# Kernel optimization log

Hardware: AMD Instinct MI355X
Metric: run time of the kernel (lower is better)

## Reference

```python
import jax, jax.numpy as jnp
import numpy as np

B, S, ENC_H, DEC_H, ATTN = 64, 2048, 512, 512, 512


def setup_inputs() -> dict:
    key = jax.random.key(0)
    k1, k2, k3, k4, k5 = jax.random.split(key, 5)
    enc_outputs = jax.random.normal(k1, (B, S, ENC_H), dtype=jnp.float32)
    dec_hidden = jax.random.normal(k2, (B, DEC_H), dtype=jnp.float32)
    # nn.Linear(in, out, bias=False): weight shape [out, in]; y = x @ W.T
    s_enc = 1.0 / np.sqrt(ENC_H)
    s_dec = 1.0 / np.sqrt(DEC_H)
    s_v = 1.0 / np.sqrt(ATTN)
    W_enc = jax.random.uniform(k3, (ATTN, ENC_H), minval=-s_enc, maxval=s_enc, dtype=jnp.float32)
    W_dec = jax.random.uniform(k4, (ATTN, DEC_H), minval=-s_dec, maxval=s_dec, dtype=jnp.float32)
    v = jax.random.uniform(k5, (1, ATTN), minval=-s_v, maxval=s_v, dtype=jnp.float32)
    return {"enc_outputs": enc_outputs, "dec_hidden": dec_hidden,
            "W_enc": W_enc, "W_dec": W_dec, "v": v}


def reference(enc_outputs, dec_hidden, W_enc, W_dec, v):
    # enc_proj: [B,S,A], dec_proj: [B,1,A]
    enc_proj = jnp.einsum('bse,ae->bsa', enc_outputs, W_enc)
    dec_proj = jnp.einsum('bd,ad->ba', dec_hidden, W_dec)[:, None, :]
    score = jnp.einsum('bsa,a->bs', jnp.tanh(enc_proj + dec_proj), v[0])  # [B,S]
    attn_weights = jax.nn.softmax(score, axis=1)
    context = jnp.einsum('bs,bse->be', attn_weights, enc_outputs)  # [B,ENC_H]
    return (context, attn_weights)
```

## Files before the change

### kernel.cpp

```cpp
#include <hip/hip_runtime.h>
#include <hip/hip_bf16.h>

#define B_N 64
#define S_N 2048
#define E_N 512
#define A_N 512

typedef __bf16 bf16x8 __attribute__((ext_vector_type(8)));
typedef float  f32x4  __attribute__((ext_vector_type(4)));

__device__ __forceinline__ unsigned int f2bfu(float f) {
  return (unsigned int)__builtin_bit_cast(unsigned short, (__bf16)f);
}

__global__ __launch_bounds__(256) void k_pack(const float* __restrict__ W,
                                              unsigned short* __restrict__ Wp) {
  const int pk = blockIdx.x * 256 + threadIdx.x;
  const int l = pk & 63, k32 = (pk >> 6) & 15, c = pk >> 10;
  const int ln = l & 15, q = l >> 4;
  const int a = c * 16 + ln, k = k32 * 32 + q * 8;
  const float* src = W + (size_t)a * E_N + k;
  const float4 u = *(const float4*)src;
  const float4 w = *(const float4*)(src + 4);
  uint4 o;
  o.x = f2bfu(u.x) | (f2bfu(u.y) << 16);
  o.y = f2bfu(u.z) | (f2bfu(u.w) << 16);
  o.z = f2bfu(w.x) | (f2bfu(w.y) << 16);
  o.w = f2bfu(w.z) | (f2bfu(w.w) << 16);
  *(uint4*)(Wp + (size_t)pk * 8) = o;
}

__global__ __launch_bounds__(256) void k_decproj(const float* __restrict__ dh,
                                                 const float* __restrict__ Wd,
                                                 float* __restrict__ decp) {
  const int b = blockIdx.x, tid = threadIdx.x;
  __shared__ float h[E_N];
  h[tid] = dh[b * E_N + tid];
  h[tid + 256] = dh[b * E_N + 256 + tid];
  __syncthreads();
  for (int a = tid; a < A_N; a += 256) {
    const float* wr = Wd + (size_t)a * E_N;
    float s = 0.f;
    #pragma unroll 8
    for (int e = 0; e < E_N; e += 4) {
      const float4 w4 = *(const float4*)(wr + e);
      s += w4.x * h[e] + w4.y * h[e + 1] + w4.z * h[e + 2] + w4.w * h[e + 3];
    }
    decp[b * A_N + a] = s;
  }
}

#define LDS_A   65536
#define RED_OFF LDS_A
#define LDS_TOT (LDS_A + 8 * 64 * 4)

__device__ __forceinline__ int a_off(int r, int kb) {
  return r * 1024 + (kb ^ ((r & 7) << 4));
}

__global__ __launch_bounds__(512, 4) void k_scores(
    const float* __restrict__ enc, const unsigned short* __restrict__ Wp,
    const float* __restrict__ decp, const float* __restrict__ vvec,
    float* __restrict__ scores) {
  __shared__ __align__(16) unsigned char lds[LDS_TOT];
  const int tid = threadIdx.x;
  const int lane = tid & 63, wv = tid >> 6, q = lane >> 4, ln = lane & 15;
  const int row0 = blockIdx.x * 64;
  const int b = row0 >> 11;
  const bf16x8* __restrict__ Wp16 = (const bf16x8*)Wp;

  float vv[4], dp[4];
  #pragma unroll
  for (int nt = 0; nt < 4; ++nt) {
    const int a = wv * 64 + nt * 16 + ln;
    vv[nt] = vvec[a];
    dp[nt] = decp[b * A_N + a];
  }

  {
    const float* srow = enc + (size_t)(row0 + wv * 8) * E_N + lane * 8;
    #pragma unroll 2
    for (int r8 = 0; r8 < 8; ++r8) {
      const float4 u = *(const float4*)(srow + (size_t)r8 * E_N);
      const float4 w = *(const float4*)(srow + (size_t)r8 * E_N + 4);
      uint4 o;
      o.x = f2bfu(u.x) | (f2bfu(u.y) << 16);
      o.y = f2bfu(u.z) | (f2bfu(u.w) << 16);
      o.z = f2bfu(w.x) | (f2bfu(w.y) << 16);
      o.w = f2bfu(w.z) | (f2bfu(w.w) << 16);
      *(uint4*)(lds + a_off(wv * 8 + r8, lane * 16)) = o;
    }
  }
  __syncthreads();

  f32x4 acc[4][4] = {};
  #pragma unroll 1
  for (int kss = 0; kss < 16; ++kss) {
    bf16x8 bfr[4], afr[4];
    #pragma unroll
    for (int nt = 0; nt < 4; ++nt)
      bfr[nt] = Wp16[(size_t)((wv * 4 + nt) * 16 + kss) * 64 + lane];
    #pragma unroll
    for (int mt = 0; mt < 4; ++mt)
      afr[mt] = *(const bf16x8*)(lds + a_off(mt * 16 + ln, kss * 64 + q * 16));
    #pragma unroll
    for (int mt = 0; mt < 4; ++mt)
      #pragma unroll
      for (int nt = 0; nt < 4; ++nt)
        acc[mt][nt] = __builtin_amdgcn_mfma_f32_16x16x32_bf16(
            afr[mt], bfr[nt], acc[mt][nt], 0, 0, 0);
  }

  float part[4][4] = {};
  #pragma unroll
  for (int mt = 0; mt < 4; ++mt)
    #pragma unroll
    for (int nt = 0; nt < 4; ++nt)
      #pragma unroll
      for (int r = 0; r < 4; ++r) {
        float x = acc[mt][nt][r] + dp[nt];
        x = fminf(9.f, fmaxf(-9.f, x));
        const float ex = __expf(2.f * x);
        part[mt][r] = fmaf(__fdividef(ex - 1.f, ex + 1.f), vv[nt], part[mt][r]);
      }
  float* red = (float*)(lds + RED_OFF);
  #pragma unroll
  for (int mt = 0; mt < 4; ++mt)
    #pragma unroll
    for (int r = 0; r < 4; ++r) {
      float s = part[mt][r];
      s += __shfl_xor(s, 1);
      s += __shfl_xor(s, 2);
      s += __shfl_xor(s, 4);
      s += __shfl_xor(s, 8);
      if (ln == 0) red[wv * 64 + mt * 16 + q * 4 + r] = s;
    }
  __syncthreads();
  if (tid < 64) {
    float s = 0.f;
    #pragma unroll
    for (int w8 = 0; w8 < 8; ++w8) s += red[w8 * 64 + tid];
    scores[row0 + tid] = s;
  }
}

__global__ __launch_bounds__(256) void k_softmax(const float* __restrict__ scores,
                                                 float* __restrict__ attn) {
  const int b = blockIdx.x, tid = threadIdx.x;
  float l[8];
  float mx = -3.4e38f;
  #pragma unroll
  for (int i = 0; i < 8; ++i) {
    l[i] = scores[b * S_N + i * 256 + tid];
    mx = fmaxf(mx, l[i]);
  }
  #pragma unroll
  for (int m = 1; m < 64; m <<= 1) mx = fmaxf(mx, __shfl_xor(mx, m));
  __shared__ float sred[8];
  if ((tid & 63) == 0) sred[tid >> 6] = mx;
  __syncthreads();
  mx = fmaxf(fmaxf(sred[0], sred[1]), fmaxf(sred[2], sred[3]));
  float se = 0.f;
  #pragma unroll
  for (int i = 0; i < 8; ++i) { l[i] = __expf(l[i] - mx); se += l[i]; }
  #pragma unroll
  for (int m = 1; m < 64; m <<= 1) se += __shfl_xor(se, m);
  if ((tid & 63) == 0) sred[4 + (tid >> 6)] = se;
  __syncthreads();
  se = sred[4] + sred[5] + sred[6] + sred[7];
  const float inv = 1.f / se;
  #pragma unroll
  for (int i = 0; i < 8; ++i) attn[b * S_N + i * 256 + tid] = l[i] * inv;
}

__global__ __launch_bounds__(512) void k_context(const float* __restrict__ enc,
                                                 const float* __restrict__ attn,
                                                 float* __restrict__ ctx) {
  const int blk = blockIdx.x;
  const int b = blk >> 2, eq = blk & 3;
  const int tid = threadIdx.x;
  const int te = tid & 31, sg = tid >> 5;
  const int e0 = eq * 128 + te * 4;
  const float* ep = enc + (size_t)b * S_N * E_N + e0;
  const float* wp = attn + b * S_N;
  f32x4 acc = {0.f, 0.f, 0.f, 0.f};
  const int s0 = sg * 128;
  #pragma unroll 4
  for (int s = s0; s < s0 + 128; ++s) {
    const float w = wp[s];
    const f32x4 ev = *(const f32x4*)(ep + (size_t)s * E_N);
    acc += w * ev;
  }
  __shared__ f32x4 red[16][32];
  red[sg][te] = acc;
  __syncthreads();
  if (sg == 0) {
    f32x4 t = red[0][te];
    #pragma unroll
    for (int g = 1; g < 16; ++g) t += red[g][te];
    *(f32x4*)(ctx + (size_t)b * E_N + e0) = t;
  }
}

extern "C" void kernel_launch(void* const* d_in, const int* in_sizes, int n_in,
                              void* d_out, int out_size, void* d_ws, size_t ws_size,
                              hipStream_t stream) {
  const float* enc = (const float*)d_in[0];
  const float* dh  = (const float*)d_in[1];
  const float* We  = (const float*)d_in[2];
  const float* Wd  = (const float*)d_in[3];
  const float* v   = (const float*)d_in[4];

  float* out_ctx  = (float*)d_out;
  float* out_attn = out_ctx + B_N * E_N;

  float* scores = (float*)d_ws;
  float* decp   = scores + B_N * S_N;
  unsigned short* Wp = (unsigned short*)(decp + B_N * A_N);

  k_pack   <<<128, 256, 0, stream>>>(We, Wp);
  k_decproj<<<B_N, 256, 0, stream>>>(dh, Wd, decp);
  k_scores <<<(B_N * S_N) / 64, 512, 0, stream>>>(enc, Wp, decp, v, scores);
  k_softmax<<<B_N, 256, 0, stream>>>(scores, out_attn);
  k_context<<<B_N * 4, 512, 0, stream>>>(enc, out_attn, out_ctx);
}
```

Before: 193.4 us.

## Make score kernel persistent with W slice resident in LDS and split-A partials

```diff
diff --git a/kernel.cpp b/kernel.cpp
--- a/kernel.cpp
+++ b/kernel.cpp
@@ -5,6 +5,7 @@
 #define S_N 2048
 #define E_N 512
 #define A_N 512
+#define SPN (B_N * S_N)
 
 typedef __bf16 bf16x8 __attribute__((ext_vector_type(8)));
 typedef float  f32x4  __attribute__((ext_vector_type(4)));
@@ -50,39 +51,46 @@
   }
 }
 
-#define LDS_A   65536
-#define RED_OFF LDS_A
-#define LDS_TOT (LDS_A + 8 * 64 * 4)
+#define LDSA 65536
+#define LDSW 65536
+#define LDS2 (LDSA + LDSW + 1024)
 
 __device__ __forceinline__ int a_off(int r, int kb) {
   return r * 1024 + (kb ^ ((r & 7) << 4));
 }
 
-__global__ __launch_bounds__(512, 4) void k_scores(
+__global__ __launch_bounds__(512, 2) void k_scores(
     const float* __restrict__ enc, const unsigned short* __restrict__ Wp,
     const float* __restrict__ decp, const float* __restrict__ vvec,
-    float* __restrict__ scores) {
-  __shared__ __align__(16) unsigned char lds[LDS_TOT];
+    float* __restrict__ sp) {
+  __shared__ __align__(16) unsigned char lds[LDS2];
   const int tid = threadIdx.x;
   const int lane = tid & 63, wv = tid >> 6, q = lane >> 4, ln = lane & 15;
-  const int row0 = blockIdx.x * 64;
-  const int b = row0 >> 11;
-  const bf16x8* __restrict__ Wp16 = (const bf16x8*)Wp;
-
-  float vv[4], dp[4];
-  #pragma unroll
-  for (int nt = 0; nt < 4; ++nt) {
-    const int a = wv * 64 + nt * 16 + ln;
-    vv[nt] = vvec[a];
-    dp[nt] = decp[b * A_N + a];
-  }
+  const int wr = wv & 1, wc4 = wv >> 1;
+  const int bid = blockIdx.x;
+  const int xcd = bid & 7, slot = bid >> 3;
+  const int rg = (slot >> 3) * 8 + xcd;
+  const int c8 = slot & 7;
+  const size_t rowbase = (size_t)rg * 4096;
+  const int b0 = rg * 2;
+
+  const int col = c8 * 64 + wc4 * 16 + ln;
+  const float vvv  = vvec[col];
+  const float dpv0 = decp[b0 * A_N + col];
+  const float dpv1 = decp[(b0 + 1) * A_N + col];
 
   {
-    const float* srow = enc + (size_t)(row0 + wv * 8) * E_N + lane * 8;
+    const uint4* wsrc = (const uint4*)(Wp + (size_t)c8 * 4096 * 8);
+    uint4* wdst = (uint4*)(lds + LDSA);
+    #pragma unroll
+    for (int i = 0; i < 8; ++i) wdst[i * 512 + tid] = wsrc[i * 512 + tid];
+  }
+  {
+    const float* srow = enc + (rowbase + (size_t)wv * 8) * E_N + lane * 8;
     #pragma unroll 2
     for (int r8 = 0; r8 < 8; ++r8) {
-      const float4 u = *(const float4*)(srow + (size_t)r8 * E_N);
-      const float4 w = *(const float4*)(srow + (size_t)r8 * E_N + 4);
+      const f32x4 u = *(const f32x4*)(srow + (size_t)r8 * E_N);
+      const f32x4 w = *(const f32x4*)(srow + (size_t)r8 * E_N + 4);
       uint4 o;
       o.x = f2bfu(u.x) | (f2bfu(u.y) << 16);
       o.y = f2bfu(u.z) | (f2bfu(u.w) << 16);
@@ -93,65 +101,84 @@
   }
   __syncthreads();
 
-  f32x4 acc[4][4] = {};
-  #pragma unroll 1
-  for (int kss = 0; kss < 16; ++kss) {
-    bf16x8 bfr[4], afr[4];
-    #pragma unroll
-    for (int nt = 0; nt < 4; ++nt)
-      bfr[nt] = Wp16[(size_t)((wv * 4 + nt) * 16 + kss) * 64 + lane];
-    #pragma unroll
-    for (int mt = 0; mt < 4; ++mt)
-      afr[mt] = *(const bf16x8*)(lds + a_off(mt * 16 + ln, kss * 64 + q * 16));
-    #pragma unroll
-    for (int mt = 0; mt < 4; ++mt)
+  float* red = (float*)(lds + LDSA + LDSW);
+  const unsigned char* ldsw = lds + LDSA;
+
+  for (int j = 0; j < 64; ++j) {
+    f32x4 L[16];
+    if (j < 63) {
+      const float* nb =
+          enc + (rowbase + (size_t)(j + 1) * 64 + wv * 8) * E_N + lane * 8;
       #pragma unroll
-      for (int nt = 0; nt < 4; ++nt)
-        acc[mt][nt] = __builtin_amdgcn_mfma_f32_16x16x32_bf16(
-            afr[mt], bfr[nt], acc[mt][nt], 0, 0, 0);
-  }
-
-  float part[4][4] = {};
-  #pragma unroll
-  for (int mt = 0; mt < 4; ++mt)
-    #pragma unroll
-    for (int nt = 0; nt < 4; ++nt)
+      for (int rr = 0; rr < 8; ++rr) {
+        L[rr * 2]     = *(const f32x4*)(nb + (size_t)rr * E_N);
+        L[rr * 2 + 1] = *(const f32x4*)(nb + (size_t)rr * E_N + 4);
+      }
+    }
+    f32x4 acc[2] = {};
+    #pragma unroll 1
+    for (int kss = 0; kss < 16; ++kss) {
+      const bf16x8 bfr =
+          *(const bf16x8*)(ldsw + ((wc4 * 16 + kss) * 64 + lane) * 16);
+      const bf16x8 a0 =
+          *(const bf16x8*)(lds + a_off(wr * 32 + ln, kss * 64 + q * 16));
+      const bf16x8 a1 =
+          *(const bf16x8*)(lds + a_off(wr * 32 + 16 + ln, kss * 64 + q * 16));
+      acc[0] = __builtin_amdgcn_mfma_f32_16x16x32_bf16(a0, bfr, acc[0], 0, 0, 0);
+      acc[1] = __builtin_amdgcn_mfma_f32_16x16x32_bf16(a1, bfr, acc[1], 0, 0, 0);
+    }
+    const float dpv = (j < 32) ? dpv0 : dpv1;
+    #pragma unroll
+    for (int mt = 0; mt < 2; ++mt) {
       #pragma unroll
-      for (int r = 0; r < 4; ++r) {
-        float x = acc[mt][nt][r] + dp[nt];
+      for (int rr = 0; rr < 4; ++rr) {
+        float x = acc[mt][rr] + dpv;
         x = fminf(9.f, fmaxf(-9.f, x));
         const float ex = __expf(2.f * x);
-        part[mt][r] = fmaf(__fdividef(ex - 1.f, ex + 1.f), vv[nt], part[mt][r]);
+        float s = __fdividef(ex - 1.f, ex + 1.f) * vvv;
+        s += __shfl_xor(s, 1);
+        s += __shfl_xor(s, 2);
+        s += __shfl_xor(s, 4);
+        s += __shfl_xor(s, 8);
+        if (ln == 0) red[wv * 32 + mt * 16 + q * 4 + rr] = s;
       }
-  float* red = (float*)(lds + RED_OFF);
-  #pragma unroll
-  for (int mt = 0; mt < 4; ++mt)
-    #pragma unroll
-    for (int r = 0; r < 4; ++r) {
-      float s = part[mt][r];
-      s += __shfl_xor(s, 1);
-      s += __shfl_xor(s, 2);
-      s += __shfl_xor(s, 4);
-      s += __shfl_xor(s, 8);
-      if (ln == 0) red[wv * 64 + mt * 16 + q * 4 + r] = s;
-    }
-  __syncthreads();
-  if (tid < 64) {
-    float s = 0.f;
-    #pragma unroll
-    for (int w8 = 0; w8 < 8; ++w8) s += red[w8 * 64 + tid];
-    scores[row0 + tid] = s;
-  }
-}
-
-__global__ __launch_bounds__(256) void k_softmax(const float* __restrict__ scores,
+    }
+    __syncthreads();
+    if (j < 63) {
+      #pragma unroll
+      for (int rr = 0; rr < 8; ++rr) {
+        uint4 o;
+        o.x = f2bfu(L[rr * 2].x)     | (f2bfu(L[rr * 2].y)     << 16);
+        o.y = f2bfu(L[rr * 2].z)     | (f2bfu(L[rr * 2].w)     << 16);
+        o.z = f2bfu(L[rr * 2 + 1].x) | (f2bfu(L[rr * 2 + 1].y) << 16);
+        o.w = f2bfu(L[rr * 2 + 1].z) | (f2bfu(L[rr * 2 + 1].w) << 16);
+        *(uint4*)(lds + a_off(wv * 8 + rr, lane * 16)) = o;
+      }
+    }
+    if (tid < 64) {
+      const int wr_ = tid >> 5, l32 = tid & 31;
+      const float s = red[(0 * 2 + wr_) * 32 + l32] +
+                      red[(1 * 2 + wr_) * 32 + l32] +
+                      red[(2 * 2 + wr_) * 32 + l32] +
+                      red[(3 * 2 + wr_) * 32 + l32];
+      sp[(size_t)c8 * SPN + rowbase + (size_t)j * 64 + tid] = s;
+    }
+    __syncthreads();
+  }
+}
+
+__global__ __launch_bounds__(256) void k_softmax(const float* __restrict__ sp,
                                                  float* __restrict__ attn) {
   const int b = blockIdx.x, tid = threadIdx.x;
   float l[8];
   float mx = -3.4e38f;
   #pragma unroll
   for (int i = 0; i < 8; ++i) {
-    l[i] = scores[b * S_N + i * 256 + tid];
+    const size_t idx = (size_t)b * S_N + i * 256 + tid;
+    float s = 0.f;
+    #pragma unroll
+    for (int c = 0; c < 8; ++c) s += sp[(size_t)c * SPN + idx];
+    l[i] = s;
     mx = fmaxf(mx, l[i]);
   }
   #pragma unroll
@@ -214,13 +241,13 @@
   float* out_ctx  = (float*)d_out;
   float* out_attn = out_ctx + B_N * E_N;
 
-  float* scores = (float*)d_ws;
-  float* decp   = scores + B_N * S_N;
+  float* sp   = (float*)d_ws;
+  float* decp = sp + 8 * SPN;
   unsigned short* Wp = (unsigned short*)(decp + B_N * A_N);
 
   k_pack   <<<128, 256, 0, stream>>>(We, Wp);
   k_decproj<<<B_N, 256, 0, stream>>>(dh, Wd, decp);
-  k_scores <<<(B_N * S_N) / 64, 512, 0, stream>>>(enc, Wp, decp, v, scores);
-  k_softmax<<<B_N, 256, 0, stream>>>(scores, out_attn);
+  k_scores <<<256, 512, 0, stream>>>(enc, Wp, decp, v, sp);
+  k_softmax<<<B_N, 256, 0, stream>>>(sp, out_attn);
   k_context<<<B_N * 4, 512, 0, stream>>>(enc, out_attn, out_ctx);
 }
```

New measurement: 381.6 us. 1.97x slower.

## Split fused score kernel into GEMM writing bf16 projection and separate tanh-reduce kernel

Applied to the files above, without the earlier changes.

```diff
diff --git a/kernel.cpp b/kernel.cpp
--- a/kernel.cpp
+++ b/kernel.cpp
@@ -5,12 +5,26 @@
 #define S_N 2048
 #define E_N 512
 #define A_N 512
+#define SPN (B_N * S_N)
 
 typedef __bf16 bf16x8 __attribute__((ext_vector_type(8)));
 typedef float  f32x4  __attribute__((ext_vector_type(4)));
 
 __device__ __forceinline__ unsigned int f2bfu(float f) {
   return (unsigned int)__builtin_bit_cast(unsigned short, (__bf16)f);
+}
+
+__device__ __forceinline__ float bflo(unsigned int u) {
+  return __builtin_bit_cast(float, u << 16);
+}
+__device__ __forceinline__ float bfhi(unsigned int u) {
+  return __builtin_bit_cast(float, u & 0xffff0000u);
+}
+
+__device__ __forceinline__ float tanh_term(float x) {
+  x = fminf(9.f, fmaxf(-9.f, x));
+  const float ex = __expf(2.f * x);
+  return __fdividef(ex - 1.f, ex + 1.f);
 }
 
 __global__ __launch_bounds__(256) void k_pack(const float* __restrict__ W,
@@ -51,38 +65,27 @@
 }
 
 #define LDS_A   65536
-#define RED_OFF LDS_A
-#define LDS_TOT (LDS_A + 8 * 64 * 4)
+#define LDS_TOT LDS_A
 
 __device__ __forceinline__ int a_off(int r, int kb) {
   return r * 1024 + (kb ^ ((r & 7) << 4));
 }
 
-__global__ __launch_bounds__(512, 4) void k_scores(
+__global__ __launch_bounds__(512, 4) void k_gemm(
     const float* __restrict__ enc, const unsigned short* __restrict__ Wp,
-    const float* __restrict__ decp, const float* __restrict__ vvec,
-    float* __restrict__ scores) {
+    unsigned short* __restrict__ P) {
   __shared__ __align__(16) unsigned char lds[LDS_TOT];
   const int tid = threadIdx.x;
   const int lane = tid & 63, wv = tid >> 6, q = lane >> 4, ln = lane & 15;
   const int row0 = blockIdx.x * 64;
-  const int b = row0 >> 11;
   const bf16x8* __restrict__ Wp16 = (const bf16x8*)Wp;
-
-  float vv[4], dp[4];
-  #pragma unroll
-  for (int nt = 0; nt < 4; ++nt) {
-    const int a = wv * 64 + nt * 16 + ln;
-    vv[nt] = vvec[a];
-    dp[nt] = decp[b * A_N + a];
-  }
 
   {
     const float* srow = enc + (size_t)(row0 + wv * 8) * E_N + lane * 8;
     #pragma unroll 2
     for (int r8 = 0; r8 < 8; ++r8) {
-      const float4 u = *(const float4*)(srow + (size_t)r8 * E_N);
-      const float4 w = *(const float4*)(srow + (size_t)r8 * E_N + 4);
+      const f32x4 u = *(const f32x4*)(srow + (size_t)r8 * E_N);
+      const f32x4 w = *(const f32x4*)(srow + (size_t)r8 * E_N + 4);
       uint4 o;
       o.x = f2bfu(u.x) | (f2bfu(u.y) << 16);
       o.y = f2bfu(u.z) | (f2bfu(u.w) << 16);
@@ -93,13 +96,14 @@
   }
   __syncthreads();
 
+  const bf16x8* __restrict__ wb = Wp16 + (size_t)(wv * 4) * 1024 + lane;
   f32x4 acc[4][4] = {};
   #pragma unroll 1
   for (int kss = 0; kss < 16; ++kss) {
     bf16x8 bfr[4], afr[4];
     #pragma unroll
     for (int nt = 0; nt < 4; ++nt)
-      bfr[nt] = Wp16[(size_t)((wv * 4 + nt) * 16 + kss) * 64 + lane];
+      bfr[nt] = wb[nt * 1024 + kss * 64];
     #pragma unroll
     for (int mt = 0; mt < 4; ++mt)
       afr[mt] = *(const bf16x8*)(lds + a_off(mt * 16 + ln, kss * 64 + q * 16));
@@ -111,36 +115,50 @@
             afr[mt], bfr[nt], acc[mt][nt], 0, 0, 0);
   }
 
-  float part[4][4] = {};
   #pragma unroll
   for (int mt = 0; mt < 4; ++mt)
     #pragma unroll
-    for (int nt = 0; nt < 4; ++nt)
+    for (int r = 0; r < 4; ++r) {
+      const size_t row = (size_t)row0 + mt * 16 + q * 4 + r;
       #pragma unroll
-      for (int r = 0; r < 4; ++r) {
-        float x = acc[mt][nt][r] + dp[nt];
-        x = fminf(9.f, fmaxf(-9.f, x));
-        const float ex = __expf(2.f * x);
-        part[mt][r] = fmaf(__fdividef(ex - 1.f, ex + 1.f), vv[nt], part[mt][r]);
-      }
-  float* red = (float*)(lds + RED_OFF);
-  #pragma unroll
-  for (int mt = 0; mt < 4; ++mt)
-    #pragma unroll
-    for (int r = 0; r < 4; ++r) {
-      float s = part[mt][r];
-      s += __shfl_xor(s, 1);
-      s += __shfl_xor(s, 2);
-      s += __shfl_xor(s, 4);
-      s += __shfl_xor(s, 8);
-      if (ln == 0) red[wv * 64 + mt * 16 + q * 4 + r] = s;
+      for (int nt = 0; nt < 4; ++nt)
+        P[row * A_N + wv * 64 + nt * 16 + ln] =
+            (unsigned short)f2bfu(acc[mt][nt][r]);
     }
-  __syncthreads();
-  if (tid < 64) {
+}
+
+__global__ __launch_bounds__(256) void k_tanh(
+    const unsigned short* __restrict__ P, const float* __restrict__ decp,
+    const float* __restrict__ vvec, float* __restrict__ scores) {
+  const int tid = threadIdx.x, wv = tid >> 6, lane = tid & 63;
+  const int gw = blockIdx.x * 4 + wv;
+  const int c0 = lane * 8;
+  const f32x4 vv0 = *(const f32x4*)(vvec + c0);
+  const f32x4 vv1 = *(const f32x4*)(vvec + c0 + 4);
+  const int b = (gw * 16) >> 11;
+  const f32x4 dp0 = *(const f32x4*)(decp + b * A_N + c0);
+  const f32x4 dp1 = *(const f32x4*)(decp + b * A_N + c0 + 4);
+
+  #pragma unroll 1
+  for (int i = 0; i < 16; ++i) {
+    const size_t row = (size_t)gw * 16 + i;
+    const uint4 pv = *(const uint4*)(P + row * A_N + c0);
     float s = 0.f;
-    #pragma unroll
-    for (int w8 = 0; w8 < 8; ++w8) s += red[w8 * 64 + tid];
-    scores[row0 + tid] = s;
+    s += tanh_term(bflo(pv.x) + dp0.x) * vv0.x;
+    s += tanh_term(bfhi(pv.x) + dp0.y) * vv0.y;
+    s += tanh_term(bflo(pv.y) + dp0.z) * vv0.z;
+    s += tanh_term(bfhi(pv.y) + dp0.w) * vv0.w;
+    s += tanh_term(bflo(pv.z) + dp1.x) * vv1.x;
+    s += tanh_term(bfhi(pv.z) + dp1.y) * vv1.y;
+    s += tanh_term(bflo(pv.w) + dp1.z) * vv1.z;
+    s += tanh_term(bfhi(pv.w) + dp1.w) * vv1.w;
+    s += __shfl_xor(s, 1);
+    s += __shfl_xor(s, 2);
+    s += __shfl_xor(s, 4);
+    s += __shfl_xor(s, 8);
+    s += __shfl_xor(s, 16);
+    s += __shfl_xor(s, 32);
+    if (lane == 0) scores[row] = s;
   }
 }
 
@@ -214,13 +232,15 @@
   float* out_ctx  = (float*)d_out;
   float* out_attn = out_ctx + B_N * E_N;
 
-  float* scores = (float*)d_ws;
-  float* decp   = scores + B_N * S_N;
+  unsigned short* P = (unsigned short*)d_ws;
+  float* scores = (float*)(P + (size_t)SPN * A_N);
+  float* decp   = scores + SPN;
   unsigned short* Wp = (unsigned short*)(decp + B_N * A_N);
 
   k_pack   <<<128, 256, 0, stream>>>(We, Wp);
   k_decproj<<<B_N, 256, 0, stream>>>(dh, Wd, decp);
-  k_scores <<<(B_N * S_N) / 64, 512, 0, stream>>>(enc, Wp, decp, v, scores);
+  k_gemm   <<<SPN / 64, 512, 0, stream>>>(enc, Wp, P);
+  k_tanh   <<<SPN / 64, 256, 0, stream>>>(P, decp, v, scores);
   k_softmax<<<B_N, 256, 0, stream>>>(scores, out_attn);
   k_context<<<B_N * 4, 512, 0, stream>>>(enc, out_attn, out_ctx);
 }
```

Result: slower. 242.1 us (+25.2%).

## Retile score GEMM into 128x128 blocks with double-buffered LDS K-pipeline

Applied to the files above, without the earlier changes.

```diff
diff --git a/kernel.cpp b/kernel.cpp
--- a/kernel.cpp
+++ b/kernel.cpp
@@ -5,23 +5,30 @@
 #define S_N 2048
 #define E_N 512
 #define A_N 512
+#define SPN (B_N * S_N)
 
 typedef __bf16 bf16x8 __attribute__((ext_vector_type(8)));
 typedef float  f32x4  __attribute__((ext_vector_type(4)));
 
 __device__ __forceinline__ unsigned int f2bfu(float f) {
   return (unsigned int)__builtin_bit_cast(unsigned short, (__bf16)f);
+}
+
+__device__ __forceinline__ float tanh_term(float x) {
+  x = fminf(9.f, fmaxf(-9.f, x));
+  const float ex = __expf(2.f * x);
+  return __fdividef(ex - 1.f, ex + 1.f);
 }
 
 __global__ __launch_bounds__(256) void k_pack(const float* __restrict__ W,
                                               unsigned short* __restrict__ Wp) {
   const int pk = blockIdx.x * 256 + threadIdx.x;
-  const int l = pk & 63, k32 = (pk >> 6) & 15, c = pk >> 10;
-  const int ln = l & 15, q = l >> 4;
-  const int a = c * 16 + ln, k = k32 * 32 + q * 8;
+  const int l = pk & 63, c = (pk >> 6) & 15, ks = (pk >> 10) & 7, cb = pk >> 13;
+  const int a = cb * 128 + (c & 7) * 16 + (l & 15);
+  const int k = ks * 64 + (c >> 3) * 32 + (l >> 4) * 8;
   const float* src = W + (size_t)a * E_N + k;
-  const float4 u = *(const float4*)src;
-  const float4 w = *(const float4*)(src + 4);
+  const f32x4 u = *(const f32x4*)src;
+  const f32x4 w = *(const f32x4*)(src + 4);
   uint4 o;
   o.x = f2bfu(u.x) | (f2bfu(u.y) << 16);
   o.y = f2bfu(u.z) | (f2bfu(u.w) << 16);
@@ -50,108 +57,133 @@
   }
 }
 
-#define LDS_A   65536
-#define RED_OFF LDS_A
-#define LDS_TOT (LDS_A + 8 * 64 * 4)
-
-__device__ __forceinline__ int a_off(int r, int kb) {
-  return r * 1024 + (kb ^ ((r & 7) << 4));
-}
-
-__global__ __launch_bounds__(512, 4) void k_scores(
+#define ABUF 16384
+
+__global__ __launch_bounds__(256) void k_scores(
     const float* __restrict__ enc, const unsigned short* __restrict__ Wp,
     const float* __restrict__ decp, const float* __restrict__ vvec,
-    float* __restrict__ scores) {
-  __shared__ __align__(16) unsigned char lds[LDS_TOT];
+    float* __restrict__ sp) {
+  __shared__ __align__(16) unsigned char lA[2 * ABUF];
+  __shared__ __align__(16) unsigned char lB[2 * ABUF];
+  __shared__ float red[4][64];
   const int tid = threadIdx.x;
   const int lane = tid & 63, wv = tid >> 6, q = lane >> 4, ln = lane & 15;
-  const int row0 = blockIdx.x * 64;
-  const int b = row0 >> 11;
-  const bf16x8* __restrict__ Wp16 = (const bf16x8*)Wp;
+  const int wr = wv & 1, wc = wv >> 1;
+  const int o = (blockIdx.x & 7) * 512 + (blockIdx.x >> 3);
+  const int rg = o >> 2, cb = o & 3;
+  const int row0 = rg * 128, b = rg >> 4;
 
   float vv[4], dp[4];
   #pragma unroll
   for (int nt = 0; nt < 4; ++nt) {
-    const int a = wv * 64 + nt * 16 + ln;
-    vv[nt] = vvec[a];
-    dp[nt] = decp[b * A_N + a];
-  }
-
-  {
-    const float* srow = enc + (size_t)(row0 + wv * 8) * E_N + lane * 8;
-    #pragma unroll 2
-    for (int r8 = 0; r8 < 8; ++r8) {
-      const float4 u = *(const float4*)(srow + (size_t)r8 * E_N);
-      const float4 w = *(const float4*)(srow + (size_t)r8 * E_N + 4);
-      uint4 o;
-      o.x = f2bfu(u.x) | (f2bfu(u.y) << 16);
-      o.y = f2bfu(u.z) | (f2bfu(u.w) << 16);
-      o.z = f2bfu(w.x) | (f2bfu(w.y) << 16);
-      o.w = f2bfu(w.z) | (f2bfu(w.w) << 16);
-      *(uint4*)(lds + a_off(wv * 8 + r8, lane * 16)) = o;
+    const int col = cb * 128 + wc * 64 + nt * 16 + ln;
+    vv[nt] = vvec[col];
+    dp[nt] = decp[b * A_N + col];
+  }
+
+  const float* pA[4];
+  const unsigned short* pB[4];
+  int w16[4];
+  #pragma unroll
+  for (int i = 0; i < 4; ++i) {
+    const int g = i * 256 + tid, c = g >> 6, l = g & 63;
+    const int row = (c & 7) * 16 + (l & 15), kof = (c >> 3) * 32 + (l >> 4) * 8;
+    pA[i] = enc + (size_t)(row0 + row) * E_N + kof;
+    pB[i] = Wp + ((size_t)(cb * 128 + c) * 64 + l) * 8;
+    w16[i] = c * 1024 + l * 16;
+  }
+
+  f32x4 La[8];
+  uint4 Lb[4];
+
+#define ISSUE(KS)                                             \
+  {                                                           \
+    _Pragma("unroll")                                         \
+    for (int i = 0; i < 4; ++i) {                             \
+      La[2 * i]     = *(const f32x4*)(pA[i] + (KS) * 64);     \
+      La[2 * i + 1] = *(const f32x4*)(pA[i] + (KS) * 64 + 4); \
+      Lb[i]         = *(const uint4*)(pB[i] + (KS) * 8192);   \
+    }                                                         \
+  }
+
+#define WRITE(DB)                                                     \
+  {                                                                   \
+    _Pragma("unroll")                                                 \
+    for (int i = 0; i < 4; ++i) {                                     \
+      uint4 oo;                                                       \
+      oo.x = f2bfu(La[2 * i].x) | (f2bfu(La[2 * i].y) << 16);         \
+      oo.y = f2bfu(La[2 * i].z) | (f2bfu(La[2 * i].w) << 16);         \
+      oo.z = f2bfu(La[2 * i + 1].x) | (f2bfu(La[2 * i + 1].y) << 16); \
+      oo.w = f2bfu(La[2 * i + 1].z) | (f2bfu(La[2 * i + 1].w) << 16); \
+      *(uint4*)(lA + (DB) * ABUF + w16[i]) = oo;                      \
+      *(uint4*)(lB + (DB) * ABUF + w16[i]) = Lb[i];                   \
+    }                                                                 \
+  }
+
+  ISSUE(0);
+  WRITE(0);
+  __syncthreads();
+
+  f32x4 acc[4][4] = {};
+  #pragma unroll 2
+  for (int ks = 0; ks < 8; ++ks) {
+    const int buf = ks & 1;
+    if (ks < 7) ISSUE(ks + 1);
+    #pragma unroll
+    for (int kt = 0; kt < 2; ++kt) {
+      bf16x8 afr[4], bfr[4];
+      #pragma unroll
+      for (int mt = 0; mt < 4; ++mt)
+        afr[mt] = *(const bf16x8*)(
+            lA + buf * ABUF + (kt * 8 + wr * 4 + mt) * 1024 + lane * 16);
+      #pragma unroll
+      for (int nt = 0; nt < 4; ++nt)
+        bfr[nt] = *(const bf16x8*)(
+            lB + buf * ABUF + (kt * 8 + wc * 4 + nt) * 1024 + lane * 16);
+      #pragma unroll
+      for (int mt = 0; mt < 4; ++mt)
+        #pragma unroll
+        for (int nt = 0; nt < 4; ++nt)
+          acc[mt][nt] = __builtin_amdgcn_mfma_f32_16x16x32_bf16(
+              afr[mt], bfr[nt], acc[mt][nt], 0, 0, 0);
     }
-  }
-  __syncthreads();
-
-  f32x4 acc[4][4] = {};
-  #pragma unroll 1
-  for (int kss = 0; kss < 16; ++kss) {
-    bf16x8 bfr[4], afr[4];
-    #pragma unroll
-    for (int nt = 0; nt < 4; ++nt)
-      bfr[nt] = Wp16[(size_t)((wv * 4 + nt) * 16 + kss) * 64 + lane];
-    #pragma unroll
-    for (int mt = 0; mt < 4; ++mt)
-      afr[mt] = *(const bf16x8*)(lds + a_off(mt * 16 + ln, kss * 64 + q * 16));
-    #pragma unroll
-    for (int mt = 0; mt < 4; ++mt)
-      #pragma unroll
-      for (int nt = 0; nt < 4; ++nt)
-        acc[mt][nt] = __builtin_amdgcn_mfma_f32_16x16x32_bf16(
-            afr[mt], bfr[nt], acc[mt][nt], 0, 0, 0);
-  }
-
-  float part[4][4] = {};
-  #pragma unroll
-  for (int mt = 0; mt < 4; ++mt)
-    #pragma unroll
-    for (int nt = 0; nt < 4; ++nt)
-      #pragma unroll
-      for (int r = 0; r < 4; ++r) {
-        float x = acc[mt][nt][r] + dp[nt];
-        x = fminf(9.f, fmaxf(-9.f, x));
-        const float ex = __expf(2.f * x);
-        part[mt][r] = fmaf(__fdividef(ex - 1.f, ex + 1.f), vv[nt], part[mt][r]);
-      }
-  float* red = (float*)(lds + RED_OFF);
-  #pragma unroll
-  for (int mt = 0; mt < 4; ++mt)
+    if (ks < 7) WRITE(buf ^ 1);
+    __syncthreads();
+  }
+
+  #pragma unroll
+  for (int mt = 0; mt < 4; ++mt) {
     #pragma unroll
     for (int r = 0; r < 4; ++r) {
-      float s = part[mt][r];
+      float s = 0.f;
+      #pragma unroll
+      for (int nt = 0; nt < 4; ++nt)
+        s = fmaf(tanh_term(acc[mt][nt][r] + dp[nt]), vv[nt], s);
       s += __shfl_xor(s, 1);
       s += __shfl_xor(s, 2);
       s += __shfl_xor(s, 4);
       s += __shfl_xor(s, 8);
-      if (ln == 0) red[wv * 64 + mt * 16 + q * 4 + r] = s;
+      if (ln == 0) red[wv][mt * 16 + q * 4 + r] = s;
     }
-  __syncthreads();
-  if (tid < 64) {
-    float s = 0.f;
-    #pragma unroll
-    for (int w8 = 0; w8 < 8; ++w8) s += red[w8 * 64 + tid];
-    scores[row0 + tid] = s;
-  }
-}
-
-__global__ __launch_bounds__(256) void k_softmax(const float* __restrict__ scores,
+  }
+  __syncthreads();
+  if (tid < 128) {
+    const int hw = tid >> 6, rl = tid & 63;
+    sp[(size_t)cb * SPN + row0 + tid] = red[hw][rl] + red[2 + hw][rl];
+  }
+#undef ISSUE
+#undef WRITE
+}
+
+__global__ __launch_bounds__(256) void k_softmax(const float* __restrict__ sp,
                                                  float* __restrict__ attn) {
   const int b = blockIdx.x, tid = threadIdx.x;
   float l[8];
   float mx = -3.4e38f;
   #pragma unroll
   for (int i = 0; i < 8; ++i) {
-    l[i] = scores[b * S_N + i * 256 + tid];
+    const size_t idx = (size_t)b * S_N + i * 256 + tid;
+    l[i] = (sp[idx] + sp[SPN + idx]) + (sp[2 * (size_t)SPN + idx] + sp[3 * (size_t)SPN + idx]);
     mx = fmaxf(mx, l[i]);
   }
   #pragma unroll
@@ -214,13 +246,13 @@
   float* out_ctx  = (float*)d_out;
   float* out_attn = out_ctx + B_N * E_N;
 
-  float* scores = (float*)d_ws;
-  float* decp   = scores + B_N * S_N;
+  float* sp   = (float*)d_ws;
+  float* decp = sp + 4 * (size_t)SPN;
   unsigned short* Wp = (unsigned short*)(decp + B_N * A_N);
 
   k_pack   <<<128, 256, 0, stream>>>(We, Wp);
   k_decproj<<<B_N, 256, 0, stream>>>(dh, Wd, decp);
-  k_scores <<<(B_N * S_N) / 64, 512, 0, stream>>>(enc, Wp, decp, v, scores);
-  k_softmax<<<B_N, 256, 0, stream>>>(scores, out_attn);
+  k_scores <<<4096, 256, 0, stream>>>(enc, Wp, decp, v, sp);
+  k_softmax<<<B_N, 256, 0, stream>>>(sp, out_attn);
   k_context<<<B_N * 4, 512, 0, stream>>>(enc, out_attn, out_ctx);
 }
```

Measured after the change: 326.1 us. 68.6% more time.
